# Kernel tuning notes

Measured on AMD Instinct MI355X. Metric: run time of the kernel, lower is better.

The kernel has to match this reference:

```python
import jax, jax.numpy as jnp
import numpy as np

B, N, F_IN, F_OUT, E = 8, 2048, 512, 256, 5
ALPHA = 0.2  # leaky relu slope
NEG = -9e15


def setup_inputs() -> dict:
    key = jax.random.key(0)
    ks = jax.random.split(key, 11)
    s_in = 1.0 / np.sqrt(F_IN)
    s_out = 1.0 / np.sqrt(F_OUT)
    s_e = 1.0 / np.sqrt(E)
    return {
        "feat": jax.random.normal(ks[0], (B, N, F_IN), jnp.float32),
        "adj": jax.random.randint(ks[1], (B, N, N), 0, 2, jnp.int32),
        "W": jax.random.normal(ks[2], (F_IN, F_OUT), jnp.float32) * s_in,
        "W_1": jax.random.normal(ks[3], (F_IN, F_OUT), jnp.float32) * s_in,
        "W_2": jax.random.normal(ks[4], (F_IN, F_OUT), jnp.float32) * s_in,
        "a_1": jax.random.normal(ks[5], (F_OUT, 1), jnp.float32) * s_out,
        "a_2": jax.random.normal(ks[6], (F_OUT, 1), jnp.float32) * s_out,
        "a_12": jax.random.normal(ks[7], (F_OUT, F_OUT), jnp.float32) * s_out,
        "L_w": jax.random.normal(ks[8], (E, F_IN), jnp.float32) * s_in,
        "R_w": jax.random.normal(ks[9], (E, F_IN), jnp.float32) * s_in,
        "B_w": jax.random.normal(ks[10], (F_OUT, E, E), jnp.float32) * s_e,
    }


def reference(feat, adj, W, W_1, W_2, a_1, a_2, a_12, L_w, R_w, B_w):
    # --- attention ---
    h = jnp.einsum('bnf,fd->bnd', feat, W)                 # [B,N,D]
    Ax = jnp.einsum('bnd,do->bno', h, a_1)[..., 0]         # [B,N] (score of target)
    Ay = jnp.einsum('bnd,do->bno', h, a_2)[..., 0]         # [B,N] (score of source)
    A_xy = jnp.einsum('bid,de,bje->bij', h, a_12, h)       # [B,N,N] bilinear term
    logits = Ax[:, None, :] + Ay[:, :, None] + A_xy        # [B,N,N]
    e = jnp.where(logits > 0, logits, ALPHA * logits)      # leaky relu
    e = jnp.where(adj > 0, e, NEG)
    attention = jax.nn.softmax(e, axis=-1)                 # dropout p=0 / eval -> identity
    # --- aggregate ---
    feat_agg = jnp.einsum('bij,bjf->bif', attention, feat) # [B,N,F_IN]
    # --- update ---
    h_1 = jnp.einsum('bnf,fd->bnd', feat, W_1)
    h_2 = jnp.einsum('bnf,fd->bnd', feat_agg, W_2)
    e1 = jnp.einsum('bnf,ef->bne', feat, L_w)              # [B,N,E]
    e2 = jnp.einsum('bnf,ef->bne', feat_agg, R_w)          # [B,N,E]
    h_12 = jnp.einsum('bni,oij,bnj->bno', e1, B_w, e2)     # [B,N,F_OUT]
    return h_1 + h_2 + h_12  # activation=None -> identity
```

## Files before the change

kernel.cpp:

```cpp
#include <hip/hip_runtime.h>
#include <hip/hip_bf16.h>

#define BB 8
#define NN 2048
#define FIN 512
#define FOUT 256
#define EE 5
#define ALPHA_ 0.2f
#define NEGV -9e15f
#define JW 512

typedef __hip_bfloat16 bf16;
typedef __bf16 bf16x8 __attribute__((ext_vector_type(8)));
typedef float f32x4 __attribute__((ext_vector_type(4)));
typedef unsigned long long u64;

__device__ __forceinline__ float bf2f(bf16 x) { return __bfloat162float(x); }
__device__ __forceinline__ bf16 f2bf(float x) { return __float2bfloat16(x); }

__device__ __forceinline__ void async16(const bf16* g, bf16* l) {
    __builtin_amdgcn_global_load_lds(
        (const __attribute__((address_space(1))) void*)g,
        (__attribute__((address_space(3))) void*)l, 16, 0, 0);
}


__global__ void split_f32_bf16(const float* __restrict__ in,
                               bf16* __restrict__ hi, bf16* __restrict__ lo) {
    long i = ((long)blockIdx.x * blockDim.x + threadIdx.x) * 8;
    float4 a = *(const float4*)(&in[i]);
    float4 b = *(const float4*)(&in[i + 4]);
    float x[8] = { a.x, a.y, a.z, a.w, b.x, b.y, b.z, b.w };
    bf16 th[8], tl[8];
    for (int k = 0; k < 8; k++) {
        th[k] = f2bf(x[k]);
        tl[k] = f2bf(x[k] - bf2f(th[k]));
    }
    *(uint4*)(&hi[i]) = *(const uint4*)th;
    *(uint4*)(&lo[i]) = *(const uint4*)tl;
}

__global__ void pack_adj(const int* __restrict__ adj, u64* __restrict__ adjm) {
    long wid = (((long)blockIdx.x * 256) + threadIdx.x) >> 6;
    int lane = threadIdx.x & 63;
    long base = wid * 256;
    for (int c = 0; c < 4; c++) {
        int a = adj[base + c * 64 + lane];
        u64 m = __ballot(a > 0);
        if (lane == 0) adjm[base / 64 + c] = m;
    }
}

__global__ void transpose_split(const float* __restrict__ in,
                                bf16* __restrict__ hi, bf16* __restrict__ lo,
                                int R, int C) {
    __shared__ bf16 th[32][33], tl[32][33];
    int c0 = blockIdx.x * 32, r0 = blockIdx.y * 32;
    int x = threadIdx.x, y = threadIdx.y;
    for (int k = 0; k < 4; k++) {
        int r = y + k * 8;
        float f = in[(long)(r0 + r) * C + c0 + x];
        bf16 h = f2bf(f);
        th[r][x] = h;
        tl[r][x] = f2bf(f - bf2f(h));
    }
    __syncthreads();
    for (int k = 0; k < 4; k++) {
        int r = y + k * 8;
        hi[(long)(c0 + r) * R + r0 + x] = th[x][r];
        lo[(long)(c0 + r) * R + r0 + x] = tl[x][r];
    }
}

__global__ void transpose_f32_bf16(const float* __restrict__ in, bf16* __restrict__ out,
                                   int R, int C, long sin_b, long sout_b) {
    __shared__ bf16 tile[32][33];
    long bi = (long)blockIdx.z * sin_b;
    long bo = (long)blockIdx.z * sout_b;
    int c0 = blockIdx.x * 32, r0 = blockIdx.y * 32;
    int x = threadIdx.x, y = threadIdx.y;
    for (int k = 0; k < 4; k++) {
        int r = y + k * 8;
        tile[r][x] = f2bf(in[bi + (long)(r0 + r) * C + c0 + x]);
    }
    __syncthreads();
    for (int k = 0; k < 4; k++) {
        int r = y + k * 8;
        out[bo + (long)(c0 + r) * R + r0 + x] = tile[x][r];
    }
}

__global__ __launch_bounds__(256) void gemm_bt_split(
        const bf16* __restrict__ Ah, const bf16* __restrict__ Al,
        const bf16* __restrict__ Bh, const bf16* __restrict__ Bl,
        bf16* __restrict__ Chi, bf16* __restrict__ Clo,
        const float* __restrict__ bias, int Nn, int K) {
    __shared__ alignas(16) bf16 Ash[128 * 32], Asl[128 * 32];
    __shared__ alignas(16) bf16 Bsh[128 * 32], Bsl[128 * 32];
    int tid = threadIdx.x;
    int lane = tid & 63, ww = tid >> 6;
    int wm = ww >> 1, wn = ww & 1;
    int quad = lane >> 4, l16 = lane & 15;
    int qx = quad ^ ((l16 >> 1) & 3);
    int sseg = (tid & 3) ^ ((tid >> 3) & 3);
    int m0 = blockIdx.x * 128, n0 = blockIdx.y * 128;
    f32x4 acc[4][4] = {};
    for (int k0 = 0; k0 < K; k0 += 32) {
#pragma unroll
        for (int i = 0; i < 2; i++) {
            int idx = tid + i * 256;
            int row = idx >> 2;
            long ao = (long)(m0 + row) * K + k0 + sseg * 8;
            long bo = (long)(n0 + row) * K + k0 + sseg * 8;
            async16(&Ah[ao], &Ash[idx * 8]);
            async16(&Al[ao], &Asl[idx * 8]);
            async16(&Bh[bo], &Bsh[idx * 8]);
            async16(&Bl[bo], &Bsl[idx * 8]);
        }
        __syncthreads();
        bf16x8 afh[4], afl[4], bfh[4], bfl[4];
        for (int mi = 0; mi < 4; mi++) {
            int so = (wm * 64 + mi * 16 + l16) * 32 + qx * 8;
            afh[mi] = *(const bf16x8*)(&Ash[so]);
            afl[mi] = *(const bf16x8*)(&Asl[so]);
        }
        for (int ni = 0; ni < 4; ni++) {
            int so = (wn * 64 + ni * 16 + l16) * 32 + qx * 8;
            bfh[ni] = *(const bf16x8*)(&Bsh[so]);
            bfl[ni] = *(const bf16x8*)(&Bsl[so]);
        }
        for (int mi = 0; mi < 4; mi++)
            for (int ni = 0; ni < 4; ni++) {
                acc[mi][ni] = __builtin_amdgcn_mfma_f32_16x16x32_bf16(afh[mi], bfh[ni], acc[mi][ni], 0, 0, 0);
                acc[mi][ni] = __builtin_amdgcn_mfma_f32_16x16x32_bf16(afh[mi], bfl[ni], acc[mi][ni], 0, 0, 0);
                acc[mi][ni] = __builtin_amdgcn_mfma_f32_16x16x32_bf16(afl[mi], bfh[ni], acc[mi][ni], 0, 0, 0);
            }
        __syncthreads();
    }
    for (int mi = 0; mi < 4; mi++)
        for (int ni = 0; ni < 4; ni++) {
            int col = n0 + wn * 64 + ni * 16 + l16;
            float bv = bias ? bias[col] : 0.f;
            for (int r = 0; r < 4; r++) {
                int row = m0 + wm * 64 + mi * 16 + quad * 4 + r;
                float v = acc[mi][ni][r] + bv;
                bf16 h = f2bf(v);
                Chi[(long)row * Nn + col] = h;
                Clo[(long)row * Nn + col] = f2bf(v - bf2f(h));
            }
        }
}

__global__ __launch_bounds__(256) void gemm_bt(
        const bf16* __restrict__ A, const bf16* __restrict__ Bt,
        bf16* __restrict__ C, int Nn, int K, long sA, long sB, long sC) {
    __shared__ alignas(16) bf16 As[128 * 32];
    __shared__ alignas(16) bf16 Bs[128 * 32];
    const bf16* Ab = A + (long)blockIdx.z * sA;
    const bf16* Bb = Bt + (long)blockIdx.z * sB;
    bf16* Cb = C + (long)blockIdx.z * sC;
    int tid = threadIdx.x;
    int lane = tid & 63, ww = tid >> 6;
    int wm = ww >> 1, wn = ww & 1;
    int quad = lane >> 4, l16 = lane & 15;
    int qx = quad ^ ((l16 >> 1) & 3);
    int sseg = (tid & 3) ^ ((tid >> 3) & 3);
    int m0 = blockIdx.x * 128, n0 = blockIdx.y * 128;
    f32x4 acc[4][4] = {};
    for (int k0 = 0; k0 < K; k0 += 32) {
#pragma unroll
        for (int i = 0; i < 2; i++) {
            int idx = tid + i * 256;
            int row = idx >> 2;
            async16(&Ab[(long)(m0 + row) * K + k0 + sseg * 8], &As[idx * 8]);
            async16(&Bb[(long)(n0 + row) * K + k0 + sseg * 8], &Bs[idx * 8]);
        }
        __syncthreads();
        bf16x8 af[4], bfr[4];
        for (int mi = 0; mi < 4; mi++)
            af[mi] = *(const bf16x8*)(&As[(wm * 64 + mi * 16 + l16) * 32 + qx * 8]);
        for (int ni = 0; ni < 4; ni++)
            bfr[ni] = *(const bf16x8*)(&Bs[(wn * 64 + ni * 16 + l16) * 32 + qx * 8]);
        for (int mi = 0; mi < 4; mi++)
            for (int ni = 0; ni < 4; ni++)
                acc[mi][ni] = __builtin_amdgcn_mfma_f32_16x16x32_bf16(
                    af[mi], bfr[ni], acc[mi][ni], 0, 0, 0);
        __syncthreads();
    }
    for (int mi = 0; mi < 4; mi++)
        for (int ni = 0; ni < 4; ni++) {
            int col = n0 + wn * 64 + ni * 16 + l16;
            for (int r = 0; r < 4; r++) {
                int row = m0 + wm * 64 + mi * 16 + quad * 4 + r;
                Cb[(long)row * Nn + col] = f2bf(acc[mi][ni][r]);
            }
        }
}

__global__ __launch_bounds__(256) void gemm_pv(
        const bf16* __restrict__ A, const bf16* __restrict__ Bt,
        bf16* __restrict__ C, const float* __restrict__ rs,
        const float* __restrict__ fin) {
    __shared__ alignas(16) bf16 As[128 * 32];
    __shared__ alignas(16) bf16 Bs[128 * 32];
    int b = blockIdx.z;
    const bf16* Ab = A + (long)b * NN * NN;
    const bf16* Bb = Bt + (long)b * FIN * NN;
    bf16* Cb = C + (long)b * NN * FIN;
    int tid = threadIdx.x;
    int lane = tid & 63, ww = tid >> 6;
    int wm = ww >> 1, wn = ww & 1;
    int quad = lane >> 4, l16 = lane & 15;
    int qx = quad ^ ((l16 >> 1) & 3);
    int sseg = (tid & 3) ^ ((tid >> 3) & 3);
    int m0 = blockIdx.x * 128, n0 = blockIdx.y * 128;
    f32x4 acc[4][4] = {};
    for (int k0 = 0; k0 < NN; k0 += 32) {
        if (k0 && !(k0 & 127)) {
            int c = k0 >> 7;
#pragma unroll
            for (int mi = 0; mi < 4; mi++) {
                float4 rv = *(const float4*)(&rs[((long)b * 16 + c) * NN
                                                 + m0 + wm * 64 + mi * 16 + quad * 4]);
#pragma unroll
                for (int ni = 0; ni < 4; ni++) {
                    acc[mi][ni][0] *= rv.x;
                    acc[mi][ni][1] *= rv.y;
                    acc[mi][ni][2] *= rv.z;
                    acc[mi][ni][3] *= rv.w;
                }
            }
        }
#pragma unroll
        for (int i = 0; i < 2; i++) {
            int idx = tid + i * 256;
            int row = idx >> 2;
            async16(&Ab[(long)(m0 + row) * NN + k0 + sseg * 8], &As[idx * 8]);
            async16(&Bb[(long)(n0 + row) * NN + k0 + sseg * 8], &Bs[idx * 8]);
        }
        __syncthreads();
        bf16x8 af[4], bfr[4];
        for (int mi = 0; mi < 4; mi++)
            af[mi] = *(const bf16x8*)(&As[(wm * 64 + mi * 16 + l16) * 32 + qx * 8]);
        for (int ni = 0; ni < 4; ni++)
            bfr[ni] = *(const bf16x8*)(&Bs[(wn * 64 + ni * 16 + l16) * 32 + qx * 8]);
        for (int mi = 0; mi < 4; mi++)
            for (int ni = 0; ni < 4; ni++)
                acc[mi][ni] = __builtin_amdgcn_mfma_f32_16x16x32_bf16(
                    af[mi], bfr[ni], acc[mi][ni], 0, 0, 0);
        __syncthreads();
    }
    for (int mi = 0; mi < 4; mi++) {
        float4 fv = *(const float4*)(&fin[(long)b * NN + m0 + wm * 64 + mi * 16 + quad * 4]);
        for (int ni = 0; ni < 4; ni++) {
            int col = n0 + wn * 64 + ni * 16 + l16;
            float fvr[4] = { fv.x, fv.y, fv.z, fv.w };
            for (int r = 0; r < 4; r++) {
                int row = m0 + wm * 64 + mi * 16 + quad * 4 + r;
                Cb[(long)row * FIN + col] = f2bf(acc[mi][ni][r] * fvr[r]);
            }
        }
    }
}

__global__ void ay_kernel(const bf16* __restrict__ hh, const bf16* __restrict__ hl,
                          const float* __restrict__ a2, float* __restrict__ Ay) {
    int lane = threadIdx.x & 63, w = threadIdx.x >> 6;
    long row = (long)blockIdx.x * 4 + w;
    float p = 0.f;
    for (int i = 0; i < 4; i++) {
        int d = i * 64 + lane;
        p += (bf2f(hh[row * FOUT + d]) + bf2f(hl[row * FOUT + d])) * a2[d];
    }
    for (int off = 32; off; off >>= 1) p += __shfl_xor(p, off);
    if (lane == 0) Ay[row] = p;
}

__global__ __launch_bounds__(256) void pass_score(
        const bf16* __restrict__ qh_, const bf16* __restrict__ ql_,
        const bf16* __restrict__ hh_, const bf16* __restrict__ hl_,
        const u64* __restrict__ adjm, const float* __restrict__ Ay,
        float* __restrict__ mpm, float* __restrict__ mpl,
        bf16* __restrict__ P) {
    __shared__ alignas(16) bf16 Hsh[3 * 128 * 32], Hsl[3 * 128 * 32];
    __shared__ alignas(16) bf16 pst[4][16 * 32];
    int tid = threadIdx.x;
    int lane = tid & 63, w = tid >> 6;
    int quad = lane >> 4, l16 = lane & 15;
    int qx = quad ^ ((l16 >> 1) & 3);
    int sseg = (tid & 3) ^ ((tid >> 3) & 3);
    int b = blockIdx.z, jz = blockIdx.y;
    int i0 = blockIdx.x * 64 + w * 16;
    long qoff = ((long)b * NN + i0) * FOUT;
    const bf16* hbh = hh_ + ((long)b * NN + (long)jz * JW) * FOUT;
    const bf16* hbl = hl_ + ((long)b * NN + (long)jz * JW) * FOUT;
    const u64* amb = adjm + ((long)b * NN + i0) * (NN / 64) + jz * (JW / 64);
    char* pwc = (char*)pst[w];

    bf16x8 qfh[8], qfl[8];
#pragma unroll
    for (int kk = 0; kk < 8; kk++) {
        qfh[kk] = *(const bf16x8*)(&qh_[qoff + (long)l16 * FOUT + kk * 32 + quad * 8]);
        qfl[kk] = *(const bf16x8*)(&ql_[qoff + (long)l16 * FOUT + kk * 32 + quad * 8]);
    }
    float ay_[4];
#pragma unroll
    for (int r = 0; r < 4; r++) ay_[r] = Ay[(long)b * NN + i0 + quad * 4 + r];

    float m_[4], l_[4];
#pragma unroll
    for (int r = 0; r < 4; r++) { m_[r] = -3.0e38f; l_[r] = 0.f; }

    auto STAGE = [&](int jc, int kk, int buf) {
#pragma unroll
        for (int i = 0; i < 2; i++) {
            int idx = tid + i * 256;
            int row = idx >> 2;
            long go = (long)(jc * 128 + row) * FOUT + kk * 32 + sseg * 8;
            async16(&hbh[go], &Hsh[buf * 4096 + idx * 8]);
            async16(&hbl[go], &Hsl[buf * 4096 + idx * 8]);
        }
    };

    f32x4 sacc[8];
#pragma unroll
    for (int ni = 0; ni < 8; ni++) sacc[ni] = (f32x4){0.f, 0.f, 0.f, 0.f};

    STAGE(0, 0, 0);
    STAGE(0, 1, 1);
    int c0 = 0;
    for (int jc = 0; jc < 4; jc++) {
        u64 am[4][2];
#pragma unroll
        for (int kk = 0; kk < 8; kk++) {
            int cur = c0 + (kk % 3);       if (cur >= 3) cur -= 3;
            int nxt = c0 + ((kk + 2) % 3); if (nxt >= 3) nxt -= 3;
            if (kk == 0) {
                if (jc == 0) asm volatile("s_waitcnt vmcnt(4)" ::: "memory");
                else         asm volatile("s_waitcnt vmcnt(12)" ::: "memory");
            } else if (kk == 1) {
                if (jc == 0) asm volatile("s_waitcnt vmcnt(12)" ::: "memory");
                else         asm volatile("s_waitcnt vmcnt(20)" ::: "memory");
            } else if (kk == 2) {
                asm volatile("s_waitcnt vmcnt(12)" ::: "memory");
            } else if (kk == 7 && jc == 3) {
                asm volatile("s_waitcnt vmcnt(0)" ::: "memory");
            } else {
                asm volatile("s_waitcnt vmcnt(4)" ::: "memory");
            }
            __builtin_amdgcn_s_barrier();
            __builtin_amdgcn_sched_barrier(0);
            if (kk < 6)       STAGE(jc, kk + 2, nxt);
            else if (jc < 3)  STAGE(jc + 1, kk - 6, nxt);
            if (kk == 0) {
#pragma unroll
                for (int r = 0; r < 4; r++) {
                    long ro = (long)(quad * 4 + r) * (NN / 64) + jc * 2;
                    am[r][0] = amb[ro + 0];
                    am[r][1] = amb[ro + 1];
                }
            }

            __builtin_amdgcn_s_setprio(1);
#pragma unroll
            for (int ni = 0; ni < 8; ni++) {
                int so = cur * 4096 + (ni * 16 + l16) * 32 + qx * 8;
                bf16x8 hfh = *(const bf16x8*)(&Hsh[so]);
                bf16x8 hfl = *(const bf16x8*)(&Hsl[so]);
                sacc[ni] = __builtin_amdgcn_mfma_f32_16x16x32_bf16(qfh[kk], hfh, sacc[ni], 0, 0, 0);
                sacc[ni] = __builtin_amdgcn_mfma_f32_16x16x32_bf16(qfh[kk], hfl, sacc[ni], 0, 0, 0);
                sacc[ni] = __builtin_amdgcn_mfma_f32_16x16x32_bf16(qfl[kk], hfh, sacc[ni], 0, 0, 0);
            }
            __builtin_amdgcn_s_setprio(0);

            if (kk == 7) {
#pragma unroll
                for (int ni = 0; ni < 8; ni++)
#pragma unroll
                    for (int r = 0; r < 4; r++) {
                        float v = sacc[ni][r] + ay_[r];
                        v = v > 0.f ? v : ALPHA_ * v;
                        int bit = (int)((am[r][ni >> 2] >> ((ni * 16 + l16) & 63)) & 1);
                        sacc[ni][r] = bit ? v : NEGV;
                    }
#pragma unroll
                for (int r = 0; r < 4; r++) {
                    float mc = -3.0e38f;
#pragma unroll
                    for (int ni = 0; ni < 8; ni++) mc = fmaxf(mc, sacc[ni][r]);
                    for (int off = 8; off; off >>= 1) mc = fmaxf(mc, __shfl_xor(mc, off));
                    float mnew = fmaxf(m_[r], mc);
                    float scale = __expf(m_[r] - mnew);
                    float ps = 0.f;
#pragma unroll
                    for (int ni = 0; ni < 8; ni++) {
                        float p = __expf(sacc[ni][r] - mnew);
                        sacc[ni][r] = p;
                        ps += p;
                    }
                    for (int off = 8; off; off >>= 1) ps += __shfl_xor(ps, off);
                    l_[r] = l_[r] * scale + ps;
                    m_[r] = mnew;
                    if (l16 == 0)
                        mpm[(((long)b * 4 + jz) * 4 + jc) * NN + i0 + quad * 4 + r] = mnew;
                }
#pragma unroll
                for (int qi = 0; qi < 4; qi++) {
#pragma unroll
                    for (int ni2 = 0; ni2 < 2; ni2++)
#pragma unroll
                        for (int r = 0; r < 4; r++) {
                            int row = quad * 4 + r;
                            int byt = (row * 64 + ni2 * 32 + l16 * 2) ^ ((row & 7) << 4);
                            *(bf16*)(pwc + byt) = f2bf(sacc[qi * 2 + ni2][r]);
                        }
                    int byt = (l16 * 64 + quad * 16) ^ ((l16 & 7) << 4);
                    uint4 v = *(const uint4*)(pwc + byt);
                    *(uint4*)(&P[((long)b * NN + i0 + l16) * NN + (long)jz * JW
                                 + jc * 128 + qi * 32 + quad * 8]) = v;
                }
#pragma unroll
                for (int ni = 0; ni < 8; ni++) sacc[ni] = (f32x4){0.f, 0.f, 0.f, 0.f};
            }
            __builtin_amdgcn_sched_barrier(0);
        }
        c0 += 2; if (c0 >= 3) c0 -= 3;
    }
    if (l16 == 0)
#pragma unroll
        for (int r = 0; r < 4; r++)
            mpl[((long)b * 4 + jz) * NN + i0 + quad * 4 + r] = l_[r];
}

__global__ void ml_merge(const float* __restrict__ mpm, const float* __restrict__ mpl,
                         float* __restrict__ rs, float* __restrict__ fin) {
    long row = (long)blockIdx.x * blockDim.x + threadIdx.x;
    long b = row / NN, n = row % NN;
    float mc[16];
#pragma unroll
    for (int c = 0; c < 16; c++) mc[c] = mpm[(b * 16 + c) * NN + n];
    float m = fmaxf(fmaxf(mc[3], mc[7]), fmaxf(mc[11], mc[15]));
    float l = 0.f;
#pragma unroll
    for (int jz = 0; jz < 4; jz++)
        l += mpl[(b * 4 + jz) * NN + n] * __expf(mc[jz * 4 + 3] - m);
    fin[row] = __expf(mc[15] - m) / l;
#pragma unroll
    for (int c = 1; c < 16; c++)
        rs[(b * 16 + c) * NN + n] = __expf(mc[c - 1] - mc[c]);
}

__global__ void e_kernel(const bf16* __restrict__ X, const float* __restrict__ Wt,
                         float* __restrict__ out) {
    int lane = threadIdx.x & 63, w = threadIdx.x >> 6;
    long row = (long)blockIdx.x * 4 + w;
    uint4 raw = *(const uint4*)(&X[row * FIN + lane * 8]);
    const bf16* xp = (const bf16*)&raw;
    float xv[8];
    for (int i = 0; i < 8; i++) xv[i] = bf2f(xp[i]);
    for (int e = 0; e < EE; e++) {
        float4 w0 = *(const float4*)(&Wt[e * FIN + lane * 8]);
        float4 w1 = *(const float4*)(&Wt[e * FIN + lane * 8 + 4]);
        float p = xv[0] * w0.x + xv[1] * w0.y + xv[2] * w0.z + xv[3] * w0.w
                + xv[4] * w1.x + xv[5] * w1.y + xv[6] * w1.z + xv[7] * w1.w;
        for (int off = 32; off; off >>= 1) p += __shfl_xor(p, off);
        if (lane == 0) out[row * EE + e] = p;
    }
}

__global__ void final_kernel(float* __restrict__ out,
                             const bf16* __restrict__ h1, const bf16* __restrict__ h2,
                             const float* __restrict__ e1, const float* __restrict__ e2,
                             const float* __restrict__ Bw) {
    long row = blockIdx.x;
    int o = threadIdx.x;
    float a[EE], c[EE];
    for (int i = 0; i < EE; i++) { a[i] = e1[row * EE + i]; c[i] = e2[row * EE + i]; }
    const float* bw = Bw + (long)o * EE * EE;
    float acc = 0.f;
    for (int i = 0; i < EE; i++)
        for (int j = 0; j < EE; j++)
            acc += bw[i * EE + j] * a[i] * c[j];
    long idx = row * FOUT + o;
    out[idx] = acc + bf2f(h1[idx]) + bf2f(h2[idx]);
}

extern "C" void kernel_launch(void* const* d_in, const int* in_sizes, int n_in,
                              void* d_out, int out_size, void* d_ws, size_t ws_size,
                              hipStream_t stream) {
    const float* feat = (const float*)d_in[0];
    const int*   adj  = (const int*)d_in[1];
    const float* W    = (const float*)d_in[2];
    const float* W1   = (const float*)d_in[3];
    const float* W2   = (const float*)d_in[4];
    const float* a1   = (const float*)d_in[5];
    const float* a2   = (const float*)d_in[6];
    const float* a12  = (const float*)d_in[7];
    const float* Lw   = (const float*)d_in[8];
    const float* Rw   = (const float*)d_in[9];
    const float* Bw   = (const float*)d_in[10];
    float* out = (float*)d_out;

    char* ws = (char*)d_ws;
    size_t off = 0;
    auto alloc = [&](size_t bytes) {
        char* p = ws + off;
        off += (bytes + 255) & ~(size_t)255;
        return p;
    };
    bf16* WTh  = (bf16*)alloc((size_t)FOUT * FIN * 2);
    bf16* WTl  = (bf16*)alloc((size_t)FOUT * FIN * 2);
    bf16* W1T  = (bf16*)alloc((size_t)FOUT * FIN * 2);
    bf16* W2T  = (bf16*)alloc((size_t)FOUT * FIN * 2);
    bf16* aTh  = (bf16*)alloc((size_t)FOUT * FOUT * 2);
    bf16* aTl  = (bf16*)alloc((size_t)FOUT * FOUT * 2);
    bf16* fh   = (bf16*)alloc((size_t)BB * NN * FIN * 2);
    bf16* fl   = (bf16*)alloc((size_t)BB * NN * FIN * 2);
    bf16* hh   = (bf16*)alloc((size_t)BB * NN * FOUT * 2);
    bf16* hl   = (bf16*)alloc((size_t)BB * NN * FOUT * 2);
    bf16* featT= (bf16*)alloc((size_t)BB * NN * FIN * 2);
    float* Ay  = (float*)alloc((size_t)BB * NN * 4);
    float* mpm = (float*)alloc((size_t)BB * 4 * 4 * NN * 4);
    float* mpl = (float*)alloc((size_t)BB * 4 * NN * 4);
    float* rs  = (float*)alloc((size_t)BB * 16 * NN * 4);
    float* fin = (float*)alloc((size_t)BB * NN * 4);
    float* e1  = (float*)alloc((size_t)BB * NN * EE * 4);
    float* e2  = (float*)alloc((size_t)BB * NN * EE * 4);
    u64* adjm  = (u64*)alloc((size_t)BB * NN * (NN / 64) * 8);
    bf16* P    = (bf16*)alloc((size_t)BB * NN * NN * 2);
    bf16* qh   = (bf16*)d_out;
    bf16* ql   = qh + (size_t)BB * NN * FOUT;
    bf16* fagg = fl;
    bf16* h1   = hh;
    bf16* h2   = hl;

    dim3 tb(32, 8, 1);
    split_f32_bf16<<<(BB * NN * FIN) / (256 * 8), 256, 0, stream>>>(feat, fh, fl);
    pack_adj<<<(BB * NN * NN) / (256 * 4), 256, 0, stream>>>(adj, adjm);
    transpose_split<<<dim3(FOUT / 32, FIN / 32, 1), tb, 0, stream>>>(W, WTh, WTl, FIN, FOUT);
    transpose_split<<<dim3(FOUT / 32, FOUT / 32, 1), tb, 0, stream>>>(a12, aTh, aTl, FOUT, FOUT);
    transpose_f32_bf16<<<dim3(FOUT / 32, FIN / 32, 1), tb, 0, stream>>>(W1, W1T, FIN, FOUT, 0, 0);
    transpose_f32_bf16<<<dim3(FOUT / 32, FIN / 32, 1), tb, 0, stream>>>(W2, W2T, FIN, FOUT, 0, 0);
    transpose_f32_bf16<<<dim3(FIN / 32, NN / 32, BB), tb, 0, stream>>>(
        feat, featT, NN, FIN, (long)NN * FIN, (long)FIN * NN);
    gemm_bt_split<<<dim3(BB * NN / 128, FOUT / 128, 1), 256, 0, stream>>>(
        fh, fl, WTh, WTl, hh, hl, nullptr, FOUT, FIN);
    ay_kernel<<<BB * NN / 4, 256, 0, stream>>>(hh, hl, a2, Ay);
    gemm_bt_split<<<dim3(BB * NN / 128, FOUT / 128, 1), 256, 0, stream>>>(
        hh, hl, aTh, aTl, qh, ql, a1, FOUT, FOUT);
    pass_score<<<dim3(NN / 64, 4, BB), 256, 0, stream>>>(
        qh, ql, hh, hl, adjm, Ay, mpm, mpl, P);
    ml_merge<<<(BB * NN) / 256, 256, 0, stream>>>(mpm, mpl, rs, fin);
    gemm_pv<<<dim3(NN / 128, FIN / 128, BB), 256, 0, stream>>>(
        P, featT, fagg, rs, fin);
    gemm_bt<<<dim3(BB * NN / 128, FOUT / 128, 1), 256, 0, stream>>>(
        fh, W1T, h1, FOUT, FIN, 0, 0, 0);
    gemm_bt<<<dim3(BB * NN / 128, FOUT / 128, 1), 256, 0, stream>>>(
        fagg, W2T, h2, FOUT, FIN, 0, 0, 0);
    e_kernel<<<BB * NN / 4, 256, 0, stream>>>(fh, Lw, e1);
    e_kernel<<<BB * NN / 4, 256, 0, stream>>>(fagg, Rw, e2);
    final_kernel<<<BB * NN, FOUT, 0, stream>>>(out, h1, h2, e1, e2, Bw);
}
```

Before: 530.2 us.

## Double-buffer GEMM LDS tiles and simplify attention score pipeline to two stages

Adds two-stage LDS double buffering with explicit vmcnt waits and barriers to gemm_bt_split, gemm_bt and gemm_pv, so the global-to-LDS loads for the next K step overlap with MFMA work on the current one. The attention score kernel goes from a three-buffer to a two-buffer prefetch and now loads the adjacency mask bits just before the softmax instead of at chunk start. Its P staging tile grows so each half of the score block is written in 64-column pieces. A shallower score pipeline and an extra barrier per step may expose more load latency there, while the GEMMs double their LDS use, which can lower occupancy.

```diff
diff --git a/kernel.cpp b/kernel.cpp
--- a/kernel.cpp
+++ b/kernel.cpp
@@ -95,8 +95,8 @@
         const bf16* __restrict__ Bh, const bf16* __restrict__ Bl,
         bf16* __restrict__ Chi, bf16* __restrict__ Clo,
         const float* __restrict__ bias, int Nn, int K) {
-    __shared__ alignas(16) bf16 Ash[128 * 32], Asl[128 * 32];
-    __shared__ alignas(16) bf16 Bsh[128 * 32], Bsl[128 * 32];
+    __shared__ alignas(16) bf16 Ash[2][128 * 32], Asl[2][128 * 32];
+    __shared__ alignas(16) bf16 Bsh[2][128 * 32], Bsl[2][128 * 32];
     int tid = threadIdx.x;
     int lane = tid & 63, ww = tid >> 6;
     int wm = ww >> 1, wn = ww & 1;
@@ -105,37 +105,57 @@
     int sseg = (tid & 3) ^ ((tid >> 3) & 3);
     int m0 = blockIdx.x * 128, n0 = blockIdx.y * 128;
     f32x4 acc[4][4] = {};
-    for (int k0 = 0; k0 < K; k0 += 32) {
+    auto STAGE = [&](int k0, int buf) {
 #pragma unroll
         for (int i = 0; i < 2; i++) {
             int idx = tid + i * 256;
             int row = idx >> 2;
             long ao = (long)(m0 + row) * K + k0 + sseg * 8;
             long bo = (long)(n0 + row) * K + k0 + sseg * 8;
-            async16(&Ah[ao], &Ash[idx * 8]);
-            async16(&Al[ao], &Asl[idx * 8]);
-            async16(&Bh[bo], &Bsh[idx * 8]);
-            async16(&Bl[bo], &Bsl[idx * 8]);
-        }
-        __syncthreads();
-        bf16x8 afh[4], afl[4], bfh[4], bfl[4];
-        for (int mi = 0; mi < 4; mi++) {
-            int so = (wm * 64 + mi * 16 + l16) * 32 + qx * 8;
-            afh[mi] = *(const bf16x8*)(&Ash[so]);
-            afl[mi] = *(const bf16x8*)(&Asl[so]);
-        }
-        for (int ni = 0; ni < 4; ni++) {
-            int so = (wn * 64 + ni * 16 + l16) * 32 + qx * 8;
-            bfh[ni] = *(const bf16x8*)(&Bsh[so]);
-            bfl[ni] = *(const bf16x8*)(&Bsl[so]);
-        }
-        for (int mi = 0; mi < 4; mi++)
+            async16(&Ah[ao], &Ash[buf][idx * 8]);
+            async16(&Al[ao], &Asl[buf][idx * 8]);
+            async16(&Bh[bo], &Bsh[buf][idx * 8]);
+            async16(&Bl[bo], &Bsl[buf][idx * 8]);
+        }
+    };
+    int nk = K / 32;
+    STAGE(0, 0);
+    for (int s = 0; s < nk; s += 2) {
+#pragma unroll
+        for (int u = 0; u < 2; u++) {
+            int step = s + u;
+            if (step + 1 < nk) STAGE((step + 1) * 32, u ^ 1);
+            if (step + 1 < nk) asm volatile("s_waitcnt vmcnt(8)" ::: "memory");
+            else               asm volatile("s_waitcnt vmcnt(0)" ::: "memory");
+            __builtin_amdgcn_s_barrier();
+            __builtin_amdgcn_sched_barrier(0);
+            __builtin_amdgcn_s_setprio(1);
+            bf16x8 afh[4], afl[4], bfh[4], bfl[4];
+#pragma unroll
+            for (int mi = 0; mi < 4; mi++) {
+                int so = (wm * 64 + mi * 16 + l16) * 32 + qx * 8;
+                afh[mi] = *(const bf16x8*)(&Ash[u][so]);
+                afl[mi] = *(const bf16x8*)(&Asl[u][so]);
+            }
+#pragma unroll
             for (int ni = 0; ni < 4; ni++) {
-                acc[mi][ni] = __builtin_amdgcn_mfma_f32_16x16x32_bf16(afh[mi], bfh[ni], acc[mi][ni], 0, 0, 0);
-                acc[mi][ni] = __builtin_amdgcn_mfma_f32_16x16x32_bf16(afh[mi], bfl[ni], acc[mi][ni], 0, 0, 0);
-                acc[mi][ni] = __builtin_amdgcn_mfma_f32_16x16x32_bf16(afl[mi], bfh[ni], acc[mi][ni], 0, 0, 0);
-            }
-        __syncthreads();
+                int so = (wn * 64 + ni * 16 + l16) * 32 + qx * 8;
+                bfh[ni] = *(const bf16x8*)(&Bsh[u][so]);
+                bfl[ni] = *(const bf16x8*)(&Bsl[u][so]);
+            }
+#pragma unroll
+            for (int mi = 0; mi < 4; mi++)
+#pragma unroll
+                for (int ni = 0; ni < 4; ni++) {
+                    acc[mi][ni] = __builtin_amdgcn_mfma_f32_16x16x32_bf16(afh[mi], bfh[ni], acc[mi][ni], 0, 0, 0);
+                    acc[mi][ni] = __builtin_amdgcn_mfma_f32_16x16x32_bf16(afh[mi], bfl[ni], acc[mi][ni], 0, 0, 0);
+                    acc[mi][ni] = __builtin_amdgcn_mfma_f32_16x16x32_bf16(afl[mi], bfh[ni], acc[mi][ni], 0, 0, 0);
+                }
+            __builtin_amdgcn_s_setprio(0);
+            __builtin_amdgcn_sched_barrier(0);
+            __builtin_amdgcn_s_barrier();
+            __builtin_amdgcn_sched_barrier(0);
+        }
     }
     for (int mi = 0; mi < 4; mi++)
         for (int ni = 0; ni < 4; ni++) {
@@ -154,8 +174,8 @@
 __global__ __launch_bounds__(256) void gemm_bt(
         const bf16* __restrict__ A, const bf16* __restrict__ Bt,
         bf16* __restrict__ C, int Nn, int K, long sA, long sB, long sC) {
-    __shared__ alignas(16) bf16 As[128 * 32];
-    __shared__ alignas(16) bf16 Bs[128 * 32];
+    __shared__ alignas(16) bf16 As[2][128 * 32];
+    __shared__ alignas(16) bf16 Bs[2][128 * 32];
     const bf16* Ab = A + (long)blockIdx.z * sA;
     const bf16* Bb = Bt + (long)blockIdx.z * sB;
     bf16* Cb = C + (long)blockIdx.z * sC;
@@ -167,25 +187,45 @@
     int sseg = (tid & 3) ^ ((tid >> 3) & 3);
     int m0 = blockIdx.x * 128, n0 = blockIdx.y * 128;
     f32x4 acc[4][4] = {};
-    for (int k0 = 0; k0 < K; k0 += 32) {
+    auto STAGE = [&](int k0, int buf) {
 #pragma unroll
         for (int i = 0; i < 2; i++) {
             int idx = tid + i * 256;
             int row = idx >> 2;
-            async16(&Ab[(long)(m0 + row) * K + k0 + sseg * 8], &As[idx * 8]);
-            async16(&Bb[(long)(n0 + row) * K + k0 + sseg * 8], &Bs[idx * 8]);
-        }
-        __syncthreads();
-        bf16x8 af[4], bfr[4];
-        for (int mi = 0; mi < 4; mi++)
-            af[mi] = *(const bf16x8*)(&As[(wm * 64 + mi * 16 + l16) * 32 + qx * 8]);
-        for (int ni = 0; ni < 4; ni++)
-            bfr[ni] = *(const bf16x8*)(&Bs[(wn * 64 + ni * 16 + l16) * 32 + qx * 8]);
-        for (int mi = 0; mi < 4; mi++)
+            async16(&Ab[(long)(m0 + row) * K + k0 + sseg * 8], &As[buf][idx * 8]);
+            async16(&Bb[(long)(n0 + row) * K + k0 + sseg * 8], &Bs[buf][idx * 8]);
+        }
+    };
+    int nk = K / 32;
+    STAGE(0, 0);
+    for (int s = 0; s < nk; s += 2) {
+#pragma unroll
+        for (int u = 0; u < 2; u++) {
+            int step = s + u;
+            if (step + 1 < nk) STAGE((step + 1) * 32, u ^ 1);
+            if (step + 1 < nk) asm volatile("s_waitcnt vmcnt(4)" ::: "memory");
+            else               asm volatile("s_waitcnt vmcnt(0)" ::: "memory");
+            __builtin_amdgcn_s_barrier();
+            __builtin_amdgcn_sched_barrier(0);
+            __builtin_amdgcn_s_setprio(1);
+            bf16x8 af[4], bfr[4];
+#pragma unroll
+            for (int mi = 0; mi < 4; mi++)
+                af[mi] = *(const bf16x8*)(&As[u][(wm * 64 + mi * 16 + l16) * 32 + qx * 8]);
+#pragma unroll
             for (int ni = 0; ni < 4; ni++)
-                acc[mi][ni] = __builtin_amdgcn_mfma_f32_16x16x32_bf16(
-                    af[mi], bfr[ni], acc[mi][ni], 0, 0, 0);
-        __syncthreads();
+                bfr[ni] = *(const bf16x8*)(&Bs[u][(wn * 64 + ni * 16 + l16) * 32 + qx * 8]);
+#pragma unroll
+            for (int mi = 0; mi < 4; mi++)
+#pragma unroll
+                for (int ni = 0; ni < 4; ni++)
+                    acc[mi][ni] = __builtin_amdgcn_mfma_f32_16x16x32_bf16(
+                        af[mi], bfr[ni], acc[mi][ni], 0, 0, 0);
+            __builtin_amdgcn_s_setprio(0);
+            __builtin_amdgcn_sched_barrier(0);
+            __builtin_amdgcn_s_barrier();
+            __builtin_amdgcn_sched_barrier(0);
+        }
     }
     for (int mi = 0; mi < 4; mi++)
         for (int ni = 0; ni < 4; ni++) {
@@ -201,8 +241,8 @@
         const bf16* __restrict__ A, const bf16* __restrict__ Bt,
         bf16* __restrict__ C, const float* __restrict__ rs,
         const float* __restrict__ fin) {
-    __shared__ alignas(16) bf16 As[128 * 32];
-    __shared__ alignas(16) bf16 Bs[128 * 32];
+    __shared__ alignas(16) bf16 As[2][128 * 32];
+    __shared__ alignas(16) bf16 Bs[2][128 * 32];
     int b = blockIdx.z;
     const bf16* Ab = A + (long)b * NN * NN;
     const bf16* Bb = Bt + (long)b * FIN * NN;
@@ -215,40 +255,61 @@
     int sseg = (tid & 3) ^ ((tid >> 3) & 3);
     int m0 = blockIdx.x * 128, n0 = blockIdx.y * 128;
     f32x4 acc[4][4] = {};
-    for (int k0 = 0; k0 < NN; k0 += 32) {
-        if (k0 && !(k0 & 127)) {
-            int c = k0 >> 7;
-#pragma unroll
-            for (int mi = 0; mi < 4; mi++) {
-                float4 rv = *(const float4*)(&rs[((long)b * 16 + c) * NN
-                                                 + m0 + wm * 64 + mi * 16 + quad * 4]);
-#pragma unroll
-                for (int ni = 0; ni < 4; ni++) {
-                    acc[mi][ni][0] *= rv.x;
-                    acc[mi][ni][1] *= rv.y;
-                    acc[mi][ni][2] *= rv.z;
-                    acc[mi][ni][3] *= rv.w;
-                }
-            }
-        }
+    auto STAGE = [&](int k0, int buf) {
 #pragma unroll
         for (int i = 0; i < 2; i++) {
             int idx = tid + i * 256;
             int row = idx >> 2;
-            async16(&Ab[(long)(m0 + row) * NN + k0 + sseg * 8], &As[idx * 8]);
-            async16(&Bb[(long)(n0 + row) * NN + k0 + sseg * 8], &Bs[idx * 8]);
-        }
-        __syncthreads();
-        bf16x8 af[4], bfr[4];
-        for (int mi = 0; mi < 4; mi++)
-            af[mi] = *(const bf16x8*)(&As[(wm * 64 + mi * 16 + l16) * 32 + qx * 8]);
-        for (int ni = 0; ni < 4; ni++)
-            bfr[ni] = *(const bf16x8*)(&Bs[(wn * 64 + ni * 16 + l16) * 32 + qx * 8]);
-        for (int mi = 0; mi < 4; mi++)
+            async16(&Ab[(long)(m0 + row) * NN + k0 + sseg * 8], &As[buf][idx * 8]);
+            async16(&Bb[(long)(n0 + row) * NN + k0 + sseg * 8], &Bs[buf][idx * 8]);
+        }
+    };
+    const int nk = NN / 32;
+    STAGE(0, 0);
+    for (int s = 0; s < nk; s += 2) {
+#pragma unroll
+        for (int u = 0; u < 2; u++) {
+            int step = s + u;
+            int k0 = step * 32;
+            if (k0 && !(k0 & 127)) {
+                int c = k0 >> 7;
+#pragma unroll
+                for (int mi = 0; mi < 4; mi++) {
+                    float4 rv = *(const float4*)(&rs[((long)b * 16 + c) * NN
+                                                     + m0 + wm * 64 + mi * 16 + quad * 4]);
+#pragma unroll
+                    for (int ni = 0; ni < 4; ni++) {
+                        acc[mi][ni][0] *= rv.x;
+                        acc[mi][ni][1] *= rv.y;
+                        acc[mi][ni][2] *= rv.z;
+                        acc[mi][ni][3] *= rv.w;
+                    }
+                }
+            }
+            if (step + 1 < nk) STAGE((step + 1) * 32, u ^ 1);
+            if (step + 1 < nk) asm volatile("s_waitcnt vmcnt(4)" ::: "memory");
+            else               asm volatile("s_waitcnt vmcnt(0)" ::: "memory");
+            __builtin_amdgcn_s_barrier();
+            __builtin_amdgcn_sched_barrier(0);
+            __builtin_amdgcn_s_setprio(1);
+            bf16x8 af[4], bfr[4];
+#pragma unroll
+            for (int mi = 0; mi < 4; mi++)
+                af[mi] = *(const bf16x8*)(&As[u][(wm * 64 + mi * 16 + l16) * 32 + qx * 8]);
+#pragma unroll
             for (int ni = 0; ni < 4; ni++)
-                acc[mi][ni] = __builtin_amdgcn_mfma_f32_16x16x32_bf16(
-                    af[mi], bfr[ni], acc[mi][ni], 0, 0, 0);
-        __syncthreads();
+                bfr[ni] = *(const bf16x8*)(&Bs[u][(wn * 64 + ni * 16 + l16) * 32 + qx * 8]);
+#pragma unroll
+            for (int mi = 0; mi < 4; mi++)
+#pragma unroll
+                for (int ni = 0; ni < 4; ni++)
+                    acc[mi][ni] = __builtin_amdgcn_mfma_f32_16x16x32_bf16(
+                        af[mi], bfr[ni], acc[mi][ni], 0, 0, 0);
+            __builtin_amdgcn_s_setprio(0);
+            __builtin_amdgcn_sched_barrier(0);
+            __builtin_amdgcn_s_barrier();
+            __builtin_amdgcn_sched_barrier(0);
+        }
     }
     for (int mi = 0; mi < 4; mi++) {
         float4 fv = *(const float4*)(&fin[(long)b * NN + m0 + wm * 64 + mi * 16 + quad * 4]);
@@ -282,8 +343,8 @@
         const u64* __restrict__ adjm, const float* __restrict__ Ay,
         float* __restrict__ mpm, float* __restrict__ mpl,
         bf16* __restrict__ P) {
-    __shared__ alignas(16) bf16 Hsh[3 * 128 * 32], Hsl[3 * 128 * 32];
-    __shared__ alignas(16) bf16 pst[4][16 * 32];
+    __shared__ alignas(16) bf16 Hsh[2][128 * 32], Hsl[2][128 * 32];
+    __shared__ alignas(16) bf16 pst[4][16 * 64];
     int tid = threadIdx.x;
     int lane = tid & 63, w = tid >> 6;
     int quad = lane >> 4, l16 = lane & 15;
@@ -295,7 +356,7 @@
     const bf16* hbh = hh_ + ((long)b * NN + (long)jz * JW) * FOUT;
     const bf16* hbl = hl_ + ((long)b * NN + (long)jz * JW) * FOUT;
     const u64* amb = adjm + ((long)b * NN + i0) * (NN / 64) + jz * (JW / 64);
-    char* pwc = (char*)pst[w];
+    bf16* pw = pst[w];
 
     bf16x8 qfh[8], qfl[8];
 #pragma unroll
@@ -317,8 +378,8 @@
             int idx = tid + i * 256;
             int row = idx >> 2;
             long go = (long)(jc * 128 + row) * FOUT + kk * 32 + sseg * 8;
-            async16(&hbh[go], &Hsh[buf * 4096 + idx * 8]);
-            async16(&hbl[go], &Hsl[buf * 4096 + idx * 8]);
+            async16(&hbh[go], &Hsh[buf][idx * 8]);
+            async16(&hbl[go], &Hsl[buf][idx * 8]);
         }
     };
 
@@ -327,22 +388,15 @@
     for (int ni = 0; ni < 8; ni++) sacc[ni] = (f32x4){0.f, 0.f, 0.f, 0.f};
 
     STAGE(0, 0, 0);
-    STAGE(0, 1, 1);
-    int c0 = 0;
     for (int jc = 0; jc < 4; jc++) {
-        u64 am[4][2];
 #pragma unroll
         for (int kk = 0; kk < 8; kk++) {
-            int cur = c0 + (kk % 3);       if (cur >= 3) cur -= 3;
-            int nxt = c0 + ((kk + 2) % 3); if (nxt >= 3) nxt -= 3;
+            const int cur = kk & 1;
+            if (kk < 7)           STAGE(jc, kk + 1, cur ^ 1);
+            else if (jc < 3)      STAGE(jc + 1, 0, cur ^ 1);
             if (kk == 0) {
                 if (jc == 0) asm volatile("s_waitcnt vmcnt(4)" ::: "memory");
-                else         asm volatile("s_waitcnt vmcnt(12)" ::: "memory");
-            } else if (kk == 1) {
-                if (jc == 0) asm volatile("s_waitcnt vmcnt(12)" ::: "memory");
-                else         asm volatile("s_waitcnt vmcnt(20)" ::: "memory");
-            } else if (kk == 2) {
-                asm volatile("s_waitcnt vmcnt(12)" ::: "memory");
+                else         asm volatile("s_waitcnt vmcnt(8)" ::: "memory");
             } else if (kk == 7 && jc == 3) {
                 asm volatile("s_waitcnt vmcnt(0)" ::: "memory");
             } else {
@@ -350,23 +404,13 @@
             }
             __builtin_amdgcn_s_barrier();
             __builtin_amdgcn_sched_barrier(0);
-            if (kk < 6)       STAGE(jc, kk + 2, nxt);
-            else if (jc < 3)  STAGE(jc + 1, kk - 6, nxt);
-            if (kk == 0) {
-#pragma unroll
-                for (int r = 0; r < 4; r++) {
-                    long ro = (long)(quad * 4 + r) * (NN / 64) + jc * 2;
-                    am[r][0] = amb[ro + 0];
-                    am[r][1] = amb[ro + 1];
-                }
-            }
 
             __builtin_amdgcn_s_setprio(1);
 #pragma unroll
             for (int ni = 0; ni < 8; ni++) {
-                int so = cur * 4096 + (ni * 16 + l16) * 32 + qx * 8;
-                bf16x8 hfh = *(const bf16x8*)(&Hsh[so]);
-                bf16x8 hfl = *(const bf16x8*)(&Hsl[so]);
+                int so = (ni * 16 + l16) * 32 + qx * 8;
+                bf16x8 hfh = *(const bf16x8*)(&Hsh[cur][so]);
+                bf16x8 hfl = *(const bf16x8*)(&Hsl[cur][so]);
                 sacc[ni] = __builtin_amdgcn_mfma_f32_16x16x32_bf16(qfh[kk], hfh, sacc[ni], 0, 0, 0);
                 sacc[ni] = __builtin_amdgcn_mfma_f32_16x16x32_bf16(qfh[kk], hfl, sacc[ni], 0, 0, 0);
                 sacc[ni] = __builtin_amdgcn_mfma_f32_16x16x32_bf16(qfl[kk], hfh, sacc[ni], 0, 0, 0);
@@ -374,6 +418,12 @@
             __builtin_amdgcn_s_setprio(0);
 
             if (kk == 7) {
+                u64 am[4][2];
+#pragma unroll
+                for (int r = 0; r < 4; r++) {
+                    am[r][0] = amb[(long)(quad * 4 + r) * (NN / 64) + jc * 2 + 0];
+                    am[r][1] = amb[(long)(quad * 4 + r) * (NN / 64) + jc * 2 + 1];
+                }
 #pragma unroll
                 for (int ni = 0; ni < 8; ni++)
 #pragma unroll
@@ -405,26 +455,31 @@
                         mpm[(((long)b * 4 + jz) * 4 + jc) * NN + i0 + quad * 4 + r] = mnew;
                 }
 #pragma unroll
-                for (int qi = 0; qi < 4; qi++) {
-#pragma unroll
-                    for (int ni2 = 0; ni2 < 2; ni2++)
+                for (int h = 0; h < 2; h++) {
+#pragma unroll
+                    for (int ni = 0; ni < 4; ni++)
 #pragma unroll
                         for (int r = 0; r < 4; r++) {
                             int row = quad * 4 + r;
-                            int byt = (row * 64 + ni2 * 32 + l16 * 2) ^ ((row & 7) << 4);
-                            *(bf16*)(pwc + byt) = f2bf(sacc[qi * 2 + ni2][r]);
+                            int byt = (row * 128 + (ni * 16 + l16) * 2) ^ ((row & 7) << 4);
+                            *(bf16*)((char*)pw + byt) = f2bf(sacc[h * 4 + ni][r]);
                         }
-                    int byt = (l16 * 64 + quad * 16) ^ ((l16 & 7) << 4);
-                    uint4 v = *(const uint4*)(pwc + byt);
-                    *(uint4*)(&P[((long)b * NN + i0 + l16) * NN + (long)jz * JW
-                                 + jc * 128 + qi * 32 + quad * 8]) = v;
+#pragma unroll
+                    for (int s2 = 0; s2 < 2; s2++) {
+                        int cq = quad + s2 * 4;
+                        int byt = (l16 * 128 + cq * 16) ^ ((l16 & 7) << 4);
+                        uint4 v = *(const uint4*)((const char*)pw + byt);
+                        *(uint4*)(&P[((long)b * NN + i0 + l16) * NN + (long)jz * JW
+                                     + jc * 128 + h * 64 + cq * 8]) = v;
+                    }
                 }
 #pragma unroll
                 for (int ni = 0; ni < 8; ni++) sacc[ni] = (f32x4){0.f, 0.f, 0.f, 0.f};
             }
             __builtin_amdgcn_sched_barrier(0);
-        }
-        c0 += 2; if (c0 >= 3) c0 -= 3;
+            __builtin_amdgcn_s_barrier();
+            __builtin_amdgcn_sched_barrier(0);
+        }
     }
     if (l16 == 0)
 #pragma unroll
```

After: 521.1 us. About the same (-1.7%).
